# Kernel optimization log

Measured on AMD Instinct MI355X. Metric: run time of the kernel, lower is better.

Reference implementation:

```python
import jax, jax.numpy as jnp
import numpy as np

C = 768      # n_embd
H = 12       # n_head
L = 6        # n_layer (per stack: base and head)
BS = 256     # block_size (per-stream length t)
B = 2        # batch
VU = 512     # vocab_size_up
VD = 512     # vocab_size_down
NM = 438     # n_music


def _ln(x, g, b, eps=1e-5):
    m = jnp.mean(x, -1, keepdims=True)
    v = jnp.mean((x - m) ** 2, -1, keepdims=True)
    return (x - m) * jax.lax.rsqrt(v + eps) * g + b


def _blocks(x, p, mask):
    # p: tuple of 16 stacked [L, ...] param arrays; scan over layers
    def body(x, lp):
        g1, b1, Wq, Bq, Wk, Bk, Wv, Bv, Wo, Bo, g2, b2, Wf, Bf, Wp, Bp = lp
        Bb, T, Cc = x.shape
        D = Cc // H
        h = _ln(x, g1, b1)
        q = (h @ Wq + Bq).reshape(Bb, T, H, D).transpose(0, 2, 1, 3)
        k = (h @ Wk + Bk).reshape(Bb, T, H, D).transpose(0, 2, 1, 3)
        v = (h @ Wv + Bv).reshape(Bb, T, H, D).transpose(0, 2, 1, 3)
        att = jnp.einsum('bhid,bhjd->bhij', q, k) * (1.0 / np.sqrt(D).astype(np.float32))
        att = jnp.where(mask, att, jnp.float32(-1e9))
        att = jax.nn.softmax(att, axis=-1)
        y = jnp.einsum('bhij,bhjd->bhid', att, v).transpose(0, 2, 1, 3).reshape(Bb, T, Cc)
        x = x + y @ Wo + Bo
        h2 = _ln(x, g2, b2)
        x = x + jax.nn.gelu(h2 @ Wf + Bf, approximate=False) @ Wp + Bp
        return x, None
    x, _ = jax.lax.scan(body, x, p)
    return x


def _forward(idx_up, idx_down, cond, tok_emb_up, tok_emb_down, pos_emb, cond_w, cond_b,
             base_p, head_p, ln_f_g, ln_f_b, head_up_w, head_down_w):
    t = idx_up.shape[1]
    te = jnp.concatenate([cond @ cond_w + cond_b, tok_emb_up[idx_up], tok_emb_down[idx_down]], axis=1)
    pe = jnp.concatenate([pos_emb[:, :t], pos_emb[:, BS:BS + t], pos_emb[:, 2 * BS:2 * BS + t]], axis=1)
    x = te + pe  # [B, 3t, C]
    tril = jnp.tril(jnp.ones((t, t), bool))
    mask = jnp.tile(tril, (3, 3))[None, None]  # 3x3 tiled block-causal mask [1,1,3t,3t]
    x = _blocks(x, base_p, mask)
    x = _blocks(x, head_p, mask)
    x = _ln(x, ln_f_g, ln_f_b)
    logits_up = x[:, t:2 * t] @ head_up_w
    logits_down = x[:, 2 * t:3 * t] @ head_down_w
    return logits_up, logits_down


def setup_inputs() -> dict:
    key = jax.random.key(0)
    ks = iter(jax.random.split(key, 100))
    def nrm(shape):
        return 0.02 * jax.random.normal(next(ks), shape, jnp.float32)
    inp = {
        'idx_up': jax.random.randint(next(ks), (B, BS), 0, VU),
        'idx_down': jax.random.randint(next(ks), (B, BS), 0, VD),
        'cond': jax.random.normal(next(ks), (B, BS, NM), jnp.float32),
        'tok_emb_up': nrm((VU, C)),
        'tok_emb_down': nrm((VD, C)),
        'pos_emb': nrm((1, 3 * BS, C)),
        'cond_w': nrm((NM, C)),
        'cond_b': jnp.zeros((C,), jnp.float32),
    }
    for pre in ('base_', 'head_'):
        inp[pre + 'ln1_g'] = jnp.ones((L, C), jnp.float32)
        inp[pre + 'ln1_b'] = jnp.zeros((L, C), jnp.float32)
        inp[pre + 'wq'] = nrm((L, C, C)); inp[pre + 'bq'] = jnp.zeros((L, C), jnp.float32)
        inp[pre + 'wk'] = nrm((L, C, C)); inp[pre + 'bk'] = jnp.zeros((L, C), jnp.float32)
        inp[pre + 'wv'] = nrm((L, C, C)); inp[pre + 'bv'] = jnp.zeros((L, C), jnp.float32)
        inp[pre + 'wo'] = nrm((L, C, C)); inp[pre + 'bo'] = jnp.zeros((L, C), jnp.float32)
        inp[pre + 'ln2_g'] = jnp.ones((L, C), jnp.float32)
        inp[pre + 'ln2_b'] = jnp.zeros((L, C), jnp.float32)
        inp[pre + 'fc_w'] = nrm((L, C, 4 * C)); inp[pre + 'fc_b'] = jnp.zeros((L, 4 * C), jnp.float32)
        inp[pre + 'pr_w'] = nrm((L, 4 * C, C)); inp[pre + 'pr_b'] = jnp.zeros((L, C), jnp.float32)
    inp['ln_f_g'] = jnp.ones((C,), jnp.float32)
    inp['ln_f_b'] = jnp.zeros((C,), jnp.float32)
    inp['head_up_w'] = nrm((C, VU))
    inp['head_down_w'] = nrm((C, VD))
    return inp


def reference(idx_up, idx_down, cond, tok_emb_up, tok_emb_down, pos_emb, cond_w, cond_b,
              base_ln1_g, base_ln1_b, base_wq, base_bq, base_wk, base_bk, base_wv, base_bv,
              base_wo, base_bo, base_ln2_g, base_ln2_b, base_fc_w, base_fc_b, base_pr_w, base_pr_b,
              head_ln1_g, head_ln1_b, head_wq, head_bq, head_wk, head_bk, head_wv, head_bv,
              head_wo, head_bo, head_ln2_g, head_ln2_b, head_fc_w, head_fc_b, head_pr_w, head_pr_b,
              ln_f_g, ln_f_b, head_up_w, head_down_w):
    base_p = (base_ln1_g, base_ln1_b, base_wq, base_bq, base_wk, base_bk, base_wv, base_bv,
              base_wo, base_bo, base_ln2_g, base_ln2_b, base_fc_w, base_fc_b, base_pr_w, base_pr_b)
    head_p = (head_ln1_g, head_ln1_b, head_wq, head_bq, head_wk, head_bk, head_wv, head_bv,
              head_wo, head_bo, head_ln2_g, head_ln2_b, head_fc_w, head_fc_b, head_pr_w, head_pr_b)
    return _forward(idx_up, idx_down, cond, tok_emb_up, tok_emb_down, pos_emb, cond_w, cond_b,
                    base_p, head_p, ln_f_g, ln_f_b, head_up_w, head_down_w)
```

## Files before the change

### kernel.cpp

```cpp
#include <hip/hip_runtime.h>
#include <cmath>

typedef unsigned short u16;
typedef __bf16 bf16x8 __attribute__((ext_vector_type(8)));
typedef float f32x4 __attribute__((ext_vector_type(4)));
typedef float f32x16 __attribute__((ext_vector_type(16)));
typedef u16 u16x4 __attribute__((ext_vector_type(4)));
typedef u16 u16x2 __attribute__((ext_vector_type(2)));
typedef u16 u16x8 __attribute__((ext_vector_type(8)));

#define GLOAD16(g, l) __builtin_amdgcn_global_load_lds( \
    (const __attribute__((address_space(1))) unsigned int*)(g), \
    (__attribute__((address_space(3))) unsigned int*)(l), 16, 0, 0)

__device__ __forceinline__ u16 f2b(float f) {
  unsigned u = __builtin_bit_cast(unsigned, f);
  unsigned r = (u + 0x7fffu + ((u >> 16) & 1u)) >> 16;
  return (u16)r;
}

__device__ __forceinline__ int xcd_swz(int lin, int nwg) {
  int q = nwg >> 3, r = nwg & 7;
  int xcd = lin & 7, idx = lin >> 3;
  return xcd * q + (xcd < r ? xcd : r) + idx;
}

__device__ __forceinline__ void trans_tile(const float* __restrict__ W, u16* __restrict__ Wo,
                                           int K, int N, int Kp, int n0, int k0)
{
  __shared__ float t[32][33];
  int tx = threadIdx.x & 31, ty = threadIdx.x >> 5;
  #pragma unroll
  for (int i = 0; i < 4; ++i) {
    int k = k0 + ty + i * 8;
    t[ty + i * 8][tx] = (k < K) ? W[(long)k * N + n0 + tx] : 0.0f;
  }
  __syncthreads();
  #pragma unroll
  for (int i = 0; i < 2; ++i) {
    int p = threadIdx.x + 256 * i;
    int nl = p >> 4, kk = (p & 15) * 2;
    u16x2 o2; o2[0] = f2b(t[kk][nl]); o2[1] = f2b(t[kk + 1][nl]);
    *(u16x2*)(Wo + (long)(n0 + nl) * Kp + k0 + kk) = o2;
  }
}

__global__ __launch_bounds__(256)
void transall_k(const float* wq0, const float* wk0, const float* wv0, const float* wo0,
                const float* fc0, const float* pr0,
                const float* wq1, const float* wk1, const float* wv1, const float* wo1,
                const float* fc1, const float* pr1,
                const float* hu, const float* hd, const float* cw,
                u16* qkvt, u16* wot, u16* fct, u16* prt, u16* hutd, u16* cwt)
{
  int bid = blockIdx.x;
  const float* src; u16* dst; int K, N, Kp, t, tilesX;
  if (bid < 20736) {
    int l = bid / 1728, local = bid - l * 1728;
    int s = l / 6, li = l - s * 6;
    if (local < 432) {
      int p = local / 144; t = local - p * 144;
      const float* base = (p == 0) ? (s ? wq1 : wq0) : (p == 1) ? (s ? wk1 : wk0) : (s ? wv1 : wv0);
      src = base + (size_t)li * 768 * 768;
      dst = qkvt + (size_t)l * 2304 * 768 + (size_t)p * 768 * 768;
      K = 768; N = 768; Kp = 768; tilesX = 12;
    } else if (local < 576) {
      t = local - 432;
      src = (s ? wo1 : wo0) + (size_t)li * 768 * 768;
      dst = wot + (size_t)l * 768 * 768;
      K = 768; N = 768; Kp = 768; tilesX = 12;
    } else if (local < 1152) {
      t = local - 576;
      src = (s ? fc1 : fc0) + (size_t)li * 768 * 3072;
      dst = fct + (size_t)l * 3072 * 768;
      K = 768; N = 3072; Kp = 768; tilesX = 48;
    } else {
      t = local - 1152;
      src = (s ? pr1 : pr0) + (size_t)li * 3072 * 768;
      dst = prt + (size_t)l * 768 * 3072;
      K = 3072; N = 768; Kp = 3072; tilesX = 12;
    }
  } else {
    int e = bid - 20736;
    if (e < 96)       { t = e;       src = hu; dst = hutd;             K = 768; N = 512; Kp = 768; tilesX = 8; }
    else if (e < 192) { t = e - 96;  src = hd; dst = hutd + 512 * 768; K = 768; N = 512; Kp = 768; tilesX = 8; }
    else              { t = e - 192; src = cw; dst = cwt;              K = 438; N = 768; Kp = 448; tilesX = 12; }
  }
  int n0 = (t % tilesX) * 64, k0 = (t / tilesX) * 64;

  __shared__ float tl[64][65];
  const int tid = threadIdx.x;
  const int c4 = (tid & 15) * 4, rbase = tid >> 4;
  #pragma unroll
  for (int p = 0; p < 4; ++p) {
    int r = rbase + p * 16;
    int k = k0 + r;
    float4 v = make_float4(0.0f, 0.0f, 0.0f, 0.0f);
    if (k < K) v = *(const float4*)(src + (long)k * N + n0 + c4);
    tl[r][c4] = v.x; tl[r][c4 + 1] = v.y; tl[r][c4 + 2] = v.z; tl[r][c4 + 3] = v.w;
  }
  __syncthreads();
  const int kg = (tid & 7) * 8, nbase = tid >> 3;
  #pragma unroll
  for (int p = 0; p < 2; ++p) {
    int n = nbase + p * 32;
    u16x8 pk;
    #pragma unroll
    for (int j = 0; j < 8; ++j) pk[j] = f2b(tl[kg + j][n]);
    *(u16x8*)(dst + (long)(n0 + n) * Kp + k0 + kg) = pk;
  }
}

__global__ __launch_bounds__(256)
void transw_k(const float* __restrict__ W, u16* __restrict__ Wt,
              int K, int N, int Kp, long sIn, long sOut)
{
  int l = blockIdx.z;
  trans_tile(W + (long)l * sIn, Wt + (long)l * sOut, K, N, Kp, blockIdx.x * 32, blockIdx.y * 32);
}

__global__ __launch_bounds__(256)
void prep_k(const float* bq0, const float* bk0, const float* bv0,
            const float* bq1, const float* bk1, const float* bv1, float* qkvb,
            const float* cond, u16* cbf,
            const int* iu, const int* idn, const float* teu, const float* ted,
            const float* pe, float* x)
{
  int idx = blockIdx.x * 256 + threadIdx.x;
  if (idx < 27648) {
    int c = idx % 2304, l = idx / 2304;
    int st = l / 6, li = l % 6;
    const float* src = (c < 768) ? (st ? bq1 : bq0) : (c < 1536) ? (st ? bk1 : bk0) : (st ? bv1 : bv0);
    qkvb[idx] = src[li * 768 + (c % 768)];
  } else if (idx < 27648 + 57344) {
    int i2 = idx - 27648;
    int r = i2 / 112, kk = (i2 - r * 112) * 4;
    u16x4 pk;
    #pragma unroll
    for (int i = 0; i < 4; ++i) { int k = kk + i; pk[i] = f2b(k < 438 ? cond[r * 438 + k] : 0.0f); }
    *(u16x4*)(cbf + r * 448 + kk) = pk;
  } else if (idx < 27648 + 57344 + 196608) {
    int i3 = idx - 27648 - 57344;
    int c4 = i3 % 192; int rest = i3 / 192;
    int tt = rest % 512; int b = rest / 512;
    int i = tt & 255; int s = tt >> 8;
    int tok = s ? idn[b * 256 + i] : iu[b * 256 + i];
    const float4* src = (const float4*)(s ? (ted + (long)tok * 768) : (teu + (long)tok * 768));
    int prow = 256 + s * 256 + i;
    float4 pv = ((const float4*)(pe + (long)prow * 768))[c4];
    float4 sv = src[c4];
    float4 ov; ov.x = sv.x + pv.x; ov.y = sv.y + pv.y; ov.z = sv.z + pv.z; ov.w = sv.w + pv.w;
    ((float4*)(x + ((long)b * 768 + prow) * 768))[c4] = ov;
  }
}

template<int S, bool WX>
__global__ __launch_bounds__(256)
void lnred_k(const float* __restrict__ xin, const float* __restrict__ P,
             const float* __restrict__ bias, const float* __restrict__ gg,
             const float* __restrict__ bb, float* __restrict__ xout,
             u16* __restrict__ h)
{
  int row = blockIdx.x * 4 + (threadIdx.x >> 6);
  int lane = threadIdx.x & 63;
  long base = (long)row * 768;
  const float4* xr4 = (const float4*)(xin + base);
  float4 v[3]; float s = 0.0f;
  #pragma unroll
  for (int j = 0; j < 3; ++j) {
    int f = lane + 64 * j;
    float4 val = xr4[f];
    if (S > 0) {
      float4 bv = ((const float4*)bias)[f];
      val.x += bv.x; val.y += bv.y; val.z += bv.z; val.w += bv.w;
      #pragma unroll
      for (int si = 0; si < S; ++si) {
        float4 pv = ((const float4*)(P + (long)si * 1179648 + base))[f];
        val.x += pv.x; val.y += pv.y; val.z += pv.z; val.w += pv.w;
      }
    }
    if (WX) ((float4*)(xout + base))[f] = val;
    v[j] = val; s += val.x + val.y + val.z + val.w;
  }
  #pragma unroll
  for (int d = 1; d < 64; d <<= 1) s += __shfl_xor(s, d);
  float mean = s * (1.0f / 768.0f);
  float s2 = 0.0f;
  #pragma unroll
  for (int j = 0; j < 3; ++j) {
    float dx = v[j].x - mean, dy = v[j].y - mean, dz = v[j].z - mean, dw = v[j].w - mean;
    s2 += dx * dx + dy * dy + dz * dz + dw * dw;
  }
  #pragma unroll
  for (int d = 1; d < 64; d <<= 1) s2 += __shfl_xor(s2, d);
  float rstd = rsqrtf(s2 * (1.0f / 768.0f) + 1e-5f);
  u16* orow = h + base;
  #pragma unroll
  for (int j = 0; j < 3; ++j) {
    int f = lane + 64 * j;
    float4 gv = ((const float4*)gg)[f];
    float4 bv2 = ((const float4*)bb)[f];
    u16x4 pk;
    pk[0] = f2b((v[j].x - mean) * rstd * gv.x + bv2.x);
    pk[1] = f2b((v[j].y - mean) * rstd * gv.y + bv2.y);
    pk[2] = f2b((v[j].z - mean) * rstd * gv.z + bv2.z);
    pk[3] = f2b((v[j].w - mean) * rstd * gv.w + bv2.w);
    *(u16x4*)(orow + 4 * f) = pk;
  }
}

__global__ __launch_bounds__(256)
void headred_k(const float* __restrict__ HP, float* __restrict__ out)
{
  int i4 = blockIdx.x * 256 + threadIdx.x;
  int st = i4 >> 16, loc = i4 & 65535;
  int r = loc >> 7, c4 = loc & 127;
  const float4* basep = (const float4*)HP + (long)r * 256 + st * 128 + c4;
  float4 a = basep[0], b = basep[131072], c = basep[2 * 131072], d = basep[3 * 131072];
  float4 rr; rr.x = a.x + b.x + c.x + d.x; rr.y = a.y + b.y + c.y + d.y;
  rr.z = a.z + b.z + c.z + d.z; rr.w = a.w + b.w + c.w + d.w;
  ((float4*)out)[i4] = rr;
}

#define EPI_PLAIN 0
#define EPI_PE    1
#define EPI_QKV   2
#define EPI_GELU  4
#define EPI_PART  5
#define EPI_HEAD  6

template<int BM, int BN, int WM, int WN, int EPI, bool BIAS>
__global__ __launch_bounds__(256)
void gemm_k(const u16* __restrict__ A, const u16* __restrict__ Bt, const float* __restrict__ bias,
            float* outf, u16* outb, u16* qb, u16* kb, u16* vT, const float* aux,
            int M, int N, int Ks, int lda, int ldb, int ldc,
            int astr, int aoff, int cstr, int coff, int pstr)
{
  constexpr int NWC = BN / WN;
  constexpr int NT  = (BM / WM) * NWC * 64;
  constexpr int LCH = (BM + BN) * 8;
  constexpr int LPT = LCH / NT;
  constexpr int MR = WM / 32, NR = WN / 32;
  __shared__ alignas(16) u16 Sl[2][(BM + BN) * 64];

  const int tid = threadIdx.x;
  const int gx = gridDim.x, gy = gridDim.y;
  const int nwg = gx * gy * gridDim.z;
  const int lin = (blockIdx.z * gy + blockIdx.y) * gx + blockIdx.x;
  const int wg = xcd_swz(lin, nwg);
  const int bx = wg % gx, t1g = wg / gx;
  const int by = t1g % gy, bz = t1g / gy;
  const int m0 = bx * BM, n0 = by * BN;
  const int koff = bz * Ks;
  const int lane = tid & 63, w = tid >> 6;
  const int l31 = lane & 31, hl = lane >> 5;
  const int wr = w / NWC, wc = w % NWC;
  int aoffE = aoff;
  if constexpr (EPI == EPI_HEAD) aoffE += (by >= (int)(gy >> 1)) ? 256 : 0;

  const u16* gp[LPT]; int lbase[LPT];
  #pragma unroll
  for (int j = 0; j < LPT; ++j) {
    int c = tid + NT * j;
    int slot = c & 7;
    if (c < BM * 8) {
      int row = c >> 3;
      int se = (slot ^ (row & 7)) * 8;
      int am = m0 + row;
      gp[j] = A + (long)((am >> 8) * astr + aoffE + (am & 255)) * lda + koff + se;
    } else {
      int rb = c - BM * 8;
      int row = rb >> 3;
      int se = (slot ^ (row & 7)) * 8;
      gp[j] = Bt + (long)(n0 + row) * ldb + koff + se;
    }
    lbase[j] = w * 512 + NT * 8 * j;
  }

  int offA[4][MR], offB[4][NR];
  #pragma unroll
  for (int kst = 0; kst < 4; ++kst) {
    int s = 2 * kst + hl;
    #pragma unroll
    for (int mi = 0; mi < MR; ++mi) {
      int r = wr * WM + mi * 32 + l31;
      offA[kst][mi] = r * 128 + ((s ^ (r & 7)) << 4);
    }
    #pragma unroll
    for (int ni = 0; ni < NR; ++ni) {
      int r = wc * WN + ni * 32 + l31;
      offB[kst][ni] = BM * 128 + r * 128 + ((s ^ (r & 7)) << 4);
    }
  }

  f32x16 acc[MR][NR];
  #pragma unroll
  for (int mi = 0; mi < MR; ++mi)
  #pragma unroll
  for (int ni = 0; ni < NR; ++ni) acc[mi][ni] = f32x16{};

  auto STAGE = [&](int kt, int buf) {
    #pragma unroll
    for (int j = 0; j < LPT; ++j) GLOAD16(gp[j] + kt, &Sl[buf][lbase[j]]);
  };
  auto COMPUTE = [&](int buf) {
    const char* Sb = (const char*)&Sl[buf][0];
    #pragma unroll
    for (int kst = 0; kst < 4; ++kst) {
      bf16x8 a[MR], b[NR];
      #pragma unroll
      for (int mi = 0; mi < MR; ++mi) a[mi] = *(const bf16x8*)(Sb + offA[kst][mi]);
      #pragma unroll
      for (int ni = 0; ni < NR; ++ni) b[ni] = *(const bf16x8*)(Sb + offB[kst][ni]);
      #pragma unroll
      for (int mi = 0; mi < MR; ++mi)
      #pragma unroll
      for (int ni = 0; ni < NR; ++ni)
        acc[mi][ni] = __builtin_amdgcn_mfma_f32_32x32x16_bf16(a[mi], b[ni], acc[mi][ni], 0, 0, 0);
    }
  };

  const int nIter = Ks >> 6;
  STAGE(0, 0);
  if (nIter > 1) STAGE(64, 1);
  for (int t = 0; t < nIter; ++t) {
    if (t + 1 < nIter) {
      if constexpr (LPT == 8)      asm volatile("s_waitcnt vmcnt(8)" ::: "memory");
      else if constexpr (LPT == 6) asm volatile("s_waitcnt vmcnt(6)" ::: "memory");
      else                         asm volatile("s_waitcnt vmcnt(4)" ::: "memory");
    } else {
      asm volatile("s_waitcnt vmcnt(0)" ::: "memory");
    }
    __builtin_amdgcn_s_barrier();
    COMPUTE(t & 1);
    if (t + 2 < nIter) {
      __builtin_amdgcn_s_barrier();
      STAGE((t + 2) << 6, t & 1);
    }
  }

  #pragma unroll
  for (int mi = 0; mi < MR; ++mi)
  #pragma unroll
  for (int ni = 0; ni < NR; ++ni) {
    f32x16 a = acc[mi][ni];
    int col = n0 + wc * WN + ni * 32 + l31;
    float bv = BIAS ? bias[col] : 0.0f;
    int mlb = m0 + wr * WM + mi * 32 + 4 * hl;
    if constexpr (EPI == EPI_QKV) {
      if (col >= 1536) {
        int c2 = col - 1536, hh = c2 >> 6, dd = c2 & 63;
        #pragma unroll
        for (int q = 0; q < 4; ++q) {
          int t0r = mlb + 8 * q;
          int bb2 = t0r >= 768 ? 1 : 0;
          int t0 = t0r - bb2 * 768;
          u16x4 pk;
          #pragma unroll
          for (int r = 0; r < 4; ++r) pk[r] = f2b(a[4 * q + r] + bv);
          *(u16x4*)(vT + (long)((bb2 * 12 + hh) * 64 + dd) * 768 + t0) = pk;
        }
      } else {
        u16* dst = (col < 768) ? (qb + col) : (kb + (col - 768));
        #pragma unroll
        for (int q = 0; q < 4; ++q)
        #pragma unroll
        for (int r = 0; r < 4; ++r) {
          int row = mlb + 8 * q + r;
          dst[(long)row * 768] = f2b(a[4 * q + r] + bv);
        }
      }
    } else {
      #pragma unroll
      for (int q = 0; q < 4; ++q)
      #pragma unroll
      for (int r = 0; r < 4; ++r) {
        int rg = mlb + 8 * q + r;
        long crow = (long)(rg >> 8) * cstr + coff + (rg & 255);
        float v = a[4 * q + r] + bv;
        if (EPI == EPI_PLAIN)      outf[crow * ldc + col] = v;
        else if (EPI == EPI_PE)    outf[crow * ldc + col] = v + aux[(long)(rg & 255) * 768 + col];
        else if (EPI == EPI_PART || EPI == EPI_HEAD)
                                   outf[(long)bz * pstr + (long)rg * ldc + col] = v;
        else if (EPI == EPI_GELU)  outb[crow * ldc + col] = f2b(0.5f * v * (1.0f + erff(v * 0.70710678f)));
      }
    }
  }
}

#define MFMA_BF16 __builtin_amdgcn_mfma_f32_16x16x32_bf16
__global__ __launch_bounds__(128)
void attn_k(const u16* __restrict__ qb, const u16* __restrict__ kb,
            const u16* __restrict__ vT, u16* __restrict__ y)
{
  __shared__ alignas(16) u16 Kl[3 * 4096];
  __shared__ alignas(16) u16 Vl[3 * 4096];
  __shared__ alignas(16) u16 Pl[2][16 * 72];
  const int gx = gridDim.x, gy = gridDim.y;
  const int nwg = gx * gy;
  const int lin = blockIdx.y * gx + blockIdx.x;
  const int wg = xcd_swz(lin, nwg);
  const int qt = wg % gx, bh = wg / gx;
  const int b = bh / 12, h = bh - b * 12;
  const int tid = threadIdx.x, w = tid >> 6, lane = tid & 63, l15 = lane & 15, g = lane >> 4;
  const int qrow = qt * 32 + w * 16 + l15;
  const int qm = qrow & 255;
  const int q0 = (qt * 32) & 255;
  const unsigned nw4 = (q0 >> 6) + 1;
  const int niter = 3 * nw4;
  const u16* qp = qb + (long)(b * 768 + qrow) * 768 + h * 64;
  bf16x8 qf0 = *(const bf16x8*)(qp + 8 * g);
  bf16x8 qf1 = *(const bf16x8*)(qp + 32 + 8 * g);
  f32x4 O0{}, O1{}, O2{}, O3{};
  float m_run = -1e30f, l_run = 0.0f;

  const u16* kp[4]; const u16* vp[4]; int ldsb[4];
  #pragma unroll
  for (int j = 0; j < 4; ++j) {
    int i = tid + 128 * j;
    int r = i >> 3, sl = ((i & 7) ^ (r & 7)) * 8;
    kp[j] = kb + (long)(b * 768 + r) * 768 + h * 64 + sl;
    vp[j] = vT + (long)(bh * 64 + r) * 768 + sl;
    ldsb[j] = (w + 2 * j) * 512;
  }

  auto STAGE = [&](int kt, int q) {
    u16* kd = Kl + q * 4096; u16* vd = Vl + q * 4096;
    #pragma unroll
    for (int j = 0; j < 4; ++j) GLOAD16(kp[j] + (long)kt * 64 * 768, kd + ldsb[j]);
    #pragma unroll
    for (int j = 0; j < 4; ++j) GLOAD16(vp[j] + kt * 64, vd + ldsb[j]);
  };
  auto MAP = [&](int it) {
    unsigned sb = (unsigned)it / nw4;
    return (int)(sb * 4 + ((unsigned)it - sb * nw4));
  };

  STAGE(MAP(0), 0);
  STAGE(MAP(1), 1);
  int cur = 0;
  for (int it = 0; it < niter; ++it) {
    if (it < niter - 1) asm volatile("s_waitcnt vmcnt(8)" ::: "memory");
    else                asm volatile("s_waitcnt vmcnt(0)" ::: "memory");
    __builtin_amdgcn_s_barrier();
    if (it + 2 < niter) STAGE(MAP(it + 2), cur == 0 ? 2 : cur - 1);
    const int kt = MAP(it);
    const char* Kb = (const char*)Kl + cur * 8192;
    const char* Vb = (const char*)Vl + cur * 8192;

    f32x4 s0{}, s1{}, s2{}, s3{};
    #pragma unroll
    for (int ks = 0; ks < 2; ++ks) {
      bf16x8 qf = ks ? qf1 : qf0;
      int sb = ((4 * ks + g) ^ (l15 & 7)) << 4;
      bf16x8 k0 = *(const bf16x8*)(Kb + (0  + l15) * 128 + sb);
      bf16x8 k1 = *(const bf16x8*)(Kb + (16 + l15) * 128 + sb);
      bf16x8 k2 = *(const bf16x8*)(Kb + (32 + l15) * 128 + sb);
      bf16x8 k3 = *(const bf16x8*)(Kb + (48 + l15) * 128 + sb);
      s0 = MFMA_BF16(k0, qf, s0, 0, 0, 0);
      s1 = MFMA_BF16(k1, qf, s1, 0, 0, 0);
      s2 = MFMA_BF16(k2, qf, s2, 0, 0, 0);
      s3 = MFMA_BF16(k3, qf, s3, 0, 0, 0);
    }
    float sv[16]; float tm = -1e30f;
    #pragma unroll
    for (int mt = 0; mt < 4; ++mt) {
      f32x4 sm4 = (mt == 0) ? s0 : (mt == 1) ? s1 : (mt == 2) ? s2 : s3;
      #pragma unroll
      for (int r = 0; r < 4; ++r) {
        int kg = kt * 64 + mt * 16 + 4 * g + r;
        float val = ((kg & 255) <= qm) ? sm4[r] * 0.125f : -1e30f;
        sv[mt * 4 + r] = val; tm = fmaxf(tm, val);
      }
    }
    tm = fmaxf(tm, __shfl_xor(tm, 16));
    tm = fmaxf(tm, __shfl_xor(tm, 32));
    float mn = fmaxf(m_run, tm);
    float alpha = __expf(m_run - mn);
    float ps = 0.0f; u16 pb16[16];
    #pragma unroll
    for (int j = 0; j < 16; ++j) {
      float p = (sv[j] <= -1e29f) ? 0.0f : __expf(sv[j] - mn);
      ps += p; pb16[j] = f2b(p);
    }
    ps += __shfl_xor(ps, 16); ps += __shfl_xor(ps, 32);
    l_run = l_run * alpha + ps; m_run = mn;
    float a0 = __shfl(alpha, 4 * g + 0);
    float a1 = __shfl(alpha, 4 * g + 1);
    float a2 = __shfl(alpha, 4 * g + 2);
    float a3 = __shfl(alpha, 4 * g + 3);
    #pragma unroll
    for (int mt = 0; mt < 4; ++mt) {
      u16x4 pk; pk[0] = pb16[4*mt]; pk[1] = pb16[4*mt+1]; pk[2] = pb16[4*mt+2]; pk[3] = pb16[4*mt+3];
      *(u16x4*)((char*)&Pl[w][0] + l15 * 144 + mt * 32 + 8 * g) = pk;
    }
    O0[0] *= a0; O0[1] *= a1; O0[2] *= a2; O0[3] *= a3;
    O1[0] *= a0; O1[1] *= a1; O1[2] *= a2; O1[3] *= a3;
    O2[0] *= a0; O2[1] *= a1; O2[2] *= a2; O2[3] *= a3;
    O3[0] *= a0; O3[1] *= a1; O3[2] *= a2; O3[3] *= a3;
    asm volatile("s_waitcnt lgkmcnt(0)" ::: "memory");
    __builtin_amdgcn_sched_barrier(0);
    #pragma unroll
    for (int ks = 0; ks < 2; ++ks) {
      bf16x8 pf = *(const bf16x8*)((const char*)&Pl[w][0] + l15 * 144 + 64 * ks + 16 * g);
      int sb = ((4 * ks + g) ^ (l15 & 7)) << 4;
      bf16x8 v0 = *(const bf16x8*)(Vb + (0  + l15) * 128 + sb);
      bf16x8 v1 = *(const bf16x8*)(Vb + (16 + l15) * 128 + sb);
      bf16x8 v2 = *(const bf16x8*)(Vb + (32 + l15) * 128 + sb);
      bf16x8 v3 = *(const bf16x8*)(Vb + (48 + l15) * 128 + sb);
      O0 = MFMA_BF16(pf, v0, O0, 0, 0, 0);
      O1 = MFMA_BF16(pf, v1, O1, 0, 0, 0);
      O2 = MFMA_BF16(pf, v2, O2, 0, 0, 0);
      O3 = MFMA_BF16(pf, v3, O3, 0, 0, 0);
    }
    cur = (cur == 2) ? 0 : cur + 1;
  }
  float n0i = 1.0f / __shfl(l_run, 4 * g + 0);
  float n1i = 1.0f / __shfl(l_run, 4 * g + 1);
  float n2i = 1.0f / __shfl(l_run, 4 * g + 2);
  float n3i = 1.0f / __shfl(l_run, 4 * g + 3);
  long yr = (long)(b * 768 + qt * 32 + w * 16 + 4 * g);
  #pragma unroll
  for (int ni = 0; ni < 4; ++ni) {
    f32x4 Ov = (ni == 0) ? O0 : (ni == 1) ? O1 : (ni == 2) ? O2 : O3;
    int c = h * 64 + ni * 16 + l15;
    y[(yr + 0) * 768 + c] = f2b(Ov[0] * n0i);
    y[(yr + 1) * 768 + c] = f2b(Ov[1] * n1i);
    y[(yr + 2) * 768 + c] = f2b(Ov[2] * n2i);
    y[(yr + 3) * 768 + c] = f2b(Ov[3] * n3i);
  }
}

extern "C" void kernel_launch(void* const* d_in, const int* in_sizes, int n_in,
                              void* d_out, int out_size, void* d_ws, size_t ws_size,
                              hipStream_t stream)
{
  (void)in_sizes; (void)n_in; (void)out_size;
  auto F = [&](int i){ return (const float*)d_in[i]; };
  const int* idx_up = (const int*)d_in[0];
  const int* idx_dn = (const int*)d_in[1];
  const float* cond = F(2);
  const float* teu = F(3);
  const float* ted = F(4);
  const float* pe  = F(5);
  const float* cw  = F(6);
  const float* cb  = F(7);
  float* outp = (float*)d_out;
  char* ws = (char*)d_ws;

  size_t o = 0;
  auto take = [&](size_t bytes){ void* p = ws + o; o += bytes; return p; };
  float* x    = (float*)take(4718592);
  u16*   h    = (u16*)take(2359296);
  u16*   qbuf = (u16*)take(2359296);
  u16*   kbuf = (u16*)take(2359296);
  u16*   vT   = (u16*)take(2359296);
  u16*   y    = (u16*)take(2359296);
  u16*   fca  = (u16*)take(9437184);
  u16*   xf   = (u16*)take(2359296);
  u16*   cbf  = (u16*)take(458752);
  float* qkvb = (float*)take(110592);
  u16*   hutd = (u16*)take(1572864);
  u16*   cwt  = (u16*)take(688128);
  float* P1   = (float*)take(9437184);
  float* P2   = (float*)take(9437184);
  float* HP   = (float*)take(8388608);
  const size_t WL = 14155776;
  bool up = (ws_size >= o + 12 * WL);
  size_t nsl = up ? 12 : 1;
  u16* qkvt = (u16*)(ws + o);
  u16* wot  = qkvt + nsl * 2304 * 768;
  u16* fct  = wot  + nsl * 768 * 768;
  u16* prt  = fct  + nsl * 3072 * 768;

  auto trans = [&](const float* src, u16* dst, int K, int N, int Kp, long sIn, long sOut, int nz){
    transw_k<<<dim3(N / 32, Kp / 32, nz), dim3(256), 0, stream>>>(src, dst, K, N, Kp, sIn, sOut);
  };

  if (up) {
    transall_k<<<dim3(21012), dim3(256), 0, stream>>>(
        F(10), F(12), F(14), F(16), F(20), F(22),
        F(26), F(28), F(30), F(32), F(36), F(38),
        F(42), F(43), cw,
        qkvt, wot, fct, prt, hutd, cwt);
  } else {
    trans(F(42), hutd, 768, 512, 768, 0, 0, 1);
    trans(F(43), hutd + 512 * 768, 768, 512, 768, 0, 0, 1);
    trans(cw,    cwt, 438, 768, 448, 0, 0, 1);
  }
  prep_k<<<dim3(1100), dim3(256), 0, stream>>>(
      F(11), F(13), F(15), F(27), F(29), F(31), qkvb,
      cond, cbf, idx_up, idx_dn, teu, ted, pe, x);
  gemm_k<64, 64, 32, 32, EPI_PE, true><<<dim3(8, 12, 1), dim3(256), 0, stream>>>(cbf, cwt, cb,
      x, nullptr, nullptr, nullptr, nullptr, pe,
      512, 768, 448, 448, 448, 768, 256, 0, 768, 0, 0);

  for (int l = 0; l < 12; ++l) {
    int s = l / 6, li = l % 6;
    u16* qkvt_l = qkvt + (up ? (size_t)l : 0) * 2304 * 768;
    u16* wot_l  = wot  + (up ? (size_t)l : 0) * 768 * 768;
    u16* fct_l  = fct  + (up ? (size_t)l : 0) * 3072 * 768;
    u16* prt_l  = prt  + (up ? (size_t)l : 0) * 768 * 3072;
    if (!up) {
      for (int p = 0; p < 3; ++p)
        trans(F(8 + 16*s + 2 + 2*p) + (size_t)li*768*768, qkvt_l + (size_t)p*768*768, 768, 768, 768, 0, 0, 1);
      trans(F(8 + 16*s + 8)  + (size_t)li*768*768,  wot_l, 768, 768, 768, 0, 0, 1);
      trans(F(8 + 16*s + 12) + (size_t)li*768*3072, fct_l, 768, 3072, 768, 0, 0, 1);
      trans(F(8 + 16*s + 14) + (size_t)li*3072*768, prt_l, 3072, 768, 3072, 0, 0, 1);
    }
    if (l == 0) {
      lnred_k<0, false><<<dim3(384), dim3(256), 0, stream>>>(x, nullptr, nullptr,
          F(8+16*s+0) + (size_t)li*768, F(8+16*s+1) + (size_t)li*768, nullptr, h);
    } else {
      int ps = (l - 1) / 6, pli = (l - 1) % 6;
      lnred_k<2, true><<<dim3(384), dim3(256), 0, stream>>>(x, P2,
          F(8+16*ps+15) + (size_t)pli*768,
          F(8+16*s+0) + (size_t)li*768, F(8+16*s+1) + (size_t)li*768, x, h);
    }
    gemm_k<128, 64, 32, 64, EPI_QKV, true><<<dim3(12, 36, 1), dim3(256), 0, stream>>>(h, qkvt_l, qkvb + (size_t)l*2304,
        nullptr, nullptr, qbuf, kbuf, vT, nullptr,
        1536, 2304, 768, 768, 768, 768, 256, 0, 256, 0, 0);
    attn_k<<<dim3(24, 24), dim3(128), 0, stream>>>(qbuf, kbuf, vT, y);
    gemm_k<128, 64, 32, 64, EPI_PART, false><<<dim3(12, 12, 2), dim3(256), 0, stream>>>(y, wot_l, nullptr,
        P1, nullptr, nullptr, nullptr, nullptr, nullptr,
        1536, 768, 384, 768, 768, 768, 256, 0, 256, 0, 1179648);
    lnred_k<2, true><<<dim3(384), dim3(256), 0, stream>>>(x, P1,
        F(8+16*s+9) + (size_t)li*768,
        F(8+16*s+10) + (size_t)li*768, F(8+16*s+11) + (size_t)li*768, x, h);
    gemm_k<128, 64, 32, 64, EPI_GELU, true><<<dim3(12, 48, 1), dim3(256), 0, stream>>>(h, fct_l, F(8+16*s+13) + (size_t)li*3072,
        nullptr, fca, nullptr, nullptr, nullptr, nullptr,
        1536, 3072, 768, 768, 768, 3072, 256, 0, 256, 0, 0);
    gemm_k<128, 64, 32, 64, EPI_PART, false><<<dim3(12, 12, 2), dim3(256), 0, stream>>>(fca, prt_l, nullptr,
        P2, nullptr, nullptr, nullptr, nullptr, nullptr,
        1536, 768, 1536, 3072, 3072, 768, 256, 0, 256, 0, 1179648);
  }
  lnred_k<2, false><<<dim3(384), dim3(256), 0, stream>>>(x, P2,
      F(8+16*1+15) + (size_t)5*768, F(40), F(41), nullptr, xf);
  gemm_k<64, 64, 32, 32, EPI_HEAD, false><<<dim3(8, 16, 4), dim3(256), 0, stream>>>(xf, hutd, nullptr,
      HP, nullptr, nullptr, nullptr, nullptr, nullptr,
      512, 1024, 192, 768, 768, 1024, 768, 256, 256, 0, 524288);
  headred_k<<<dim3(512), dim3(256), 0, stream>>>(HP, outp);
}
```

Baseline: 1.227 ms.

## Fuse layernorm into following GEMMs via cooperative launch with grid sync

Merges each layernorm/residual-reduce kernel with the GEMM that consumes it into a single cooperative kernel. Each workgroup first normalizes rows, then a grid-wide sync, then runs the GEMM tile body. This cuts separate kernel launches and gaps between them. In exchange it adds the cost of a grid barrier, and cooperative launch requires all 432/576/512 workgroups to be co-resident, which constrains occupancy.

Result: slower. 3.078 ms (+150.8%).

```diff
diff --git a/kernel.cpp b/kernel.cpp
--- a/kernel.cpp
+++ b/kernel.cpp
@@ -1,5 +1,8 @@
 #include <hip/hip_runtime.h>
+#include <hip/hip_cooperative_groups.h>
 #include <cmath>
+
+namespace cg = cooperative_groups;
 
 typedef unsigned short u16;
 typedef __bf16 bf16x8 __attribute__((ext_vector_type(8)));
@@ -155,13 +158,11 @@
 }
 
 template<int S, bool WX>
-__global__ __launch_bounds__(256)
-void lnred_k(const float* __restrict__ xin, const float* __restrict__ P,
-             const float* __restrict__ bias, const float* __restrict__ gg,
-             const float* __restrict__ bb, float* __restrict__ xout,
-             u16* __restrict__ h)
-{
-  int row = blockIdx.x * 4 + (threadIdx.x >> 6);
+__device__ __forceinline__ void ln_row(int row, const float* __restrict__ xin,
+                                       const float* __restrict__ P, const float* __restrict__ bias,
+                                       const float* __restrict__ gg, const float* __restrict__ bb,
+                                       float* __restrict__ xout, u16* __restrict__ h)
+{
   int lane = threadIdx.x & 63;
   long base = (long)row * 768;
   const float4* xr4 = (const float4*)(xin + base);
@@ -230,23 +231,21 @@
 #define EPI_HEAD  6
 
 template<int BM, int BN, int WM, int WN, int EPI, bool BIAS>
-__global__ __launch_bounds__(256)
-void gemm_k(const u16* __restrict__ A, const u16* __restrict__ Bt, const float* __restrict__ bias,
-            float* outf, u16* outb, u16* qb, u16* kb, u16* vT, const float* aux,
-            int M, int N, int Ks, int lda, int ldb, int ldc,
-            int astr, int aoff, int cstr, int coff, int pstr)
+__device__ __forceinline__
+void gemm_body(u16* Sl, int lin, int gx, int gy, int nwg,
+               const u16* __restrict__ A, const u16* __restrict__ Bt, const float* __restrict__ bias,
+               float* outf, u16* outb, u16* qb, u16* kb, u16* vT, const float* aux,
+               int M, int N, int Ks, int lda, int ldb, int ldc,
+               int astr, int aoff, int cstr, int coff, int pstr)
 {
   constexpr int NWC = BN / WN;
   constexpr int NT  = (BM / WM) * NWC * 64;
   constexpr int LCH = (BM + BN) * 8;
   constexpr int LPT = LCH / NT;
   constexpr int MR = WM / 32, NR = WN / 32;
-  __shared__ alignas(16) u16 Sl[2][(BM + BN) * 64];
+  constexpr int BUFE = (BM + BN) * 64;
 
   const int tid = threadIdx.x;
-  const int gx = gridDim.x, gy = gridDim.y;
-  const int nwg = gx * gy * gridDim.z;
-  const int lin = (blockIdx.z * gy + blockIdx.y) * gx + blockIdx.x;
   const int wg = xcd_swz(lin, nwg);
   const int bx = wg % gx, t1g = wg / gx;
   const int by = t1g % gy, bz = t1g / gy;
@@ -256,7 +255,7 @@
   const int l31 = lane & 31, hl = lane >> 5;
   const int wr = w / NWC, wc = w % NWC;
   int aoffE = aoff;
-  if constexpr (EPI == EPI_HEAD) aoffE += (by >= (int)(gy >> 1)) ? 256 : 0;
+  if constexpr (EPI == EPI_HEAD) aoffE += (by >= (gy >> 1)) ? 256 : 0;
 
   const u16* gp[LPT]; int lbase[LPT];
   #pragma unroll
@@ -301,10 +300,10 @@
 
   auto STAGE = [&](int kt, int buf) {
     #pragma unroll
-    for (int j = 0; j < LPT; ++j) GLOAD16(gp[j] + kt, &Sl[buf][lbase[j]]);
+    for (int j = 0; j < LPT; ++j) GLOAD16(gp[j] + kt, Sl + buf * BUFE + lbase[j]);
   };
   auto COMPUTE = [&](int buf) {
-    const char* Sb = (const char*)&Sl[buf][0];
+    const char* Sb = (const char*)Sl + buf * BUFE * 2;
     #pragma unroll
     for (int kst = 0; kst < 4; ++kst) {
       bf16x8 a[MR], b[NR];
@@ -388,6 +387,65 @@
   }
 }
 
+template<int BM, int BN, int WM, int WN, int EPI, bool BIAS>
+__global__ __launch_bounds__(256)
+void gemm_k(const u16* __restrict__ A, const u16* __restrict__ Bt, const float* __restrict__ bias,
+            float* outf, u16* outb, u16* qb, u16* kb, u16* vT, const float* aux,
+            int M, int N, int Ks, int lda, int ldb, int ldc,
+            int astr, int aoff, int cstr, int coff, int pstr)
+{
+  __shared__ alignas(16) u16 Sl[2][(BM + BN) * 64];
+  const int gx = gridDim.x, gy = gridDim.y;
+  const int nwg = gx * gy * gridDim.z;
+  const int lin = (blockIdx.z * gy + blockIdx.y) * gx + blockIdx.x;
+  gemm_body<BM, BN, WM, WN, EPI, BIAS>(&Sl[0][0], lin, gx, gy, nwg,
+      A, Bt, bias, outf, outb, qb, kb, vT, aux,
+      M, N, Ks, lda, ldb, ldc, astr, aoff, cstr, coff, pstr);
+}
+
+template<int S, bool WX>
+__global__ __launch_bounds__(256, 3)
+void coop_qkv_k(const float* xin, const float* P, const float* pbias,
+                const float* gg, const float* bb, float* xout, u16* h,
+                const u16* Bt, const float* qbias, u16* qb, u16* kb, u16* vT)
+{
+  __shared__ alignas(16) u16 Sl[2][(128 + 64) * 64];
+  int wid = blockIdx.x * 4 + (threadIdx.x >> 6);
+  if (wid < 1536) ln_row<S, WX>(wid, xin, P, pbias, gg, bb, xout, h);
+  cg::this_grid().sync();
+  gemm_body<128, 64, 32, 64, EPI_QKV, true>(&Sl[0][0], blockIdx.x, 12, 36, 432,
+      h, Bt, qbias, nullptr, nullptr, qb, kb, vT, nullptr,
+      1536, 2304, 768, 768, 768, 768, 256, 0, 256, 0, 0);
+}
+
+__global__ __launch_bounds__(256, 3)
+void coop_fc_k(const float* xin, const float* P, const float* pbias,
+               const float* gg, const float* bb, float* xout, u16* h,
+               const u16* Bt, const float* fcbias, u16* fca)
+{
+  __shared__ alignas(16) u16 Sl[2][(128 + 64) * 64];
+  int wid = blockIdx.x * 4 + (threadIdx.x >> 6);
+  if (wid < 1536) ln_row<2, true>(wid, xin, P, pbias, gg, bb, xout, h);
+  cg::this_grid().sync();
+  gemm_body<128, 64, 32, 64, EPI_GELU, true>(&Sl[0][0], blockIdx.x, 12, 48, 576,
+      h, Bt, fcbias, nullptr, fca, nullptr, nullptr, nullptr, nullptr,
+      1536, 3072, 768, 768, 768, 3072, 256, 0, 256, 0, 0);
+}
+
+__global__ __launch_bounds__(256, 3)
+void coop_head_k(const float* xin, const float* P, const float* pbias,
+                 const float* gg, const float* bb, u16* xf,
+                 const u16* Bt, float* HP)
+{
+  __shared__ alignas(16) u16 Sl[2][(64 + 64) * 64];
+  int wid = blockIdx.x * 4 + (threadIdx.x >> 6);
+  if (wid < 1536) ln_row<2, false>(wid, xin, P, pbias, gg, bb, nullptr, xf);
+  cg::this_grid().sync();
+  gemm_body<64, 64, 32, 32, EPI_HEAD, false>(&Sl[0][0], blockIdx.x, 8, 16, 512,
+      xf, Bt, nullptr, HP, nullptr, nullptr, nullptr, nullptr, nullptr,
+      512, 1024, 192, 768, 768, 1024, 768, 256, 256, 0, 524288);
+}
+
 #define MFMA_BF16 __builtin_amdgcn_mfma_f32_16x16x32_bf16
 __global__ __launch_bounds__(128)
 void attn_k(const u16* __restrict__ qb, const u16* __restrict__ kb,
@@ -608,36 +666,47 @@
       trans(F(8 + 16*s + 12) + (size_t)li*768*3072, fct_l, 768, 3072, 768, 0, 0, 1);
       trans(F(8 + 16*s + 14) + (size_t)li*3072*768, prt_l, 3072, 768, 3072, 0, 0, 1);
     }
+    const float* g1 = F(8+16*s+0) + (size_t)li*768;
+    const float* b1 = F(8+16*s+1) + (size_t)li*768;
+    const float* qbias = qkvb + (size_t)l*2304;
     if (l == 0) {
-      lnred_k<0, false><<<dim3(384), dim3(256), 0, stream>>>(x, nullptr, nullptr,
-          F(8+16*s+0) + (size_t)li*768, F(8+16*s+1) + (size_t)li*768, nullptr, h);
+      const float* pb = nullptr;
+      void* a1[] = {(void*)&x, (void*)&P2, (void*)&pb, (void*)&g1, (void*)&b1,
+                    (void*)&x, (void*)&h, (void*)&qkvt_l, (void*)&qbias,
+                    (void*)&qbuf, (void*)&kbuf, (void*)&vT};
+      hipLaunchCooperativeKernel((const void*)coop_qkv_k<0, false>, dim3(432), dim3(256), a1, 0, stream);
     } else {
       int ps = (l - 1) / 6, pli = (l - 1) % 6;
-      lnred_k<2, true><<<dim3(384), dim3(256), 0, stream>>>(x, P2,
-          F(8+16*ps+15) + (size_t)pli*768,
-          F(8+16*s+0) + (size_t)li*768, F(8+16*s+1) + (size_t)li*768, x, h);
-    }
-    gemm_k<128, 64, 32, 64, EPI_QKV, true><<<dim3(12, 36, 1), dim3(256), 0, stream>>>(h, qkvt_l, qkvb + (size_t)l*2304,
-        nullptr, nullptr, qbuf, kbuf, vT, nullptr,
-        1536, 2304, 768, 768, 768, 768, 256, 0, 256, 0, 0);
+      const float* pb = F(8+16*ps+15) + (size_t)pli*768;
+      void* a1[] = {(void*)&x, (void*)&P2, (void*)&pb, (void*)&g1, (void*)&b1,
+                    (void*)&x, (void*)&h, (void*)&qkvt_l, (void*)&qbias,
+                    (void*)&qbuf, (void*)&kbuf, (void*)&vT};
+      hipLaunchCooperativeKernel((const void*)coop_qkv_k<2, true>, dim3(432), dim3(256), a1, 0, stream);
+    }
     attn_k<<<dim3(24, 24), dim3(128), 0, stream>>>(qbuf, kbuf, vT, y);
     gemm_k<128, 64, 32, 64, EPI_PART, false><<<dim3(12, 12, 2), dim3(256), 0, stream>>>(y, wot_l, nullptr,
         P1, nullptr, nullptr, nullptr, nullptr, nullptr,
         1536, 768, 384, 768, 768, 768, 256, 0, 256, 0, 1179648);
-    lnred_k<2, true><<<dim3(384), dim3(256), 0, stream>>>(x, P1,
-        F(8+16*s+9) + (size_t)li*768,
-        F(8+16*s+10) + (size_t)li*768, F(8+16*s+11) + (size_t)li*768, x, h);
-    gemm_k<128, 64, 32, 64, EPI_GELU, true><<<dim3(12, 48, 1), dim3(256), 0, stream>>>(h, fct_l, F(8+16*s+13) + (size_t)li*3072,
-        nullptr, fca, nullptr, nullptr, nullptr, nullptr,
-        1536, 3072, 768, 768, 768, 3072, 256, 0, 256, 0, 0);
+    {
+      const float* bo = F(8+16*s+9) + (size_t)li*768;
+      const float* g2 = F(8+16*s+10) + (size_t)li*768;
+      const float* b2 = F(8+16*s+11) + (size_t)li*768;
+      const float* fcb = F(8+16*s+13) + (size_t)li*3072;
+      void* a2[] = {(void*)&x, (void*)&P1, (void*)&bo, (void*)&g2, (void*)&b2,
+                    (void*)&x, (void*)&h, (void*)&fct_l, (void*)&fcb, (void*)&fca};
+      hipLaunchCooperativeKernel((const void*)coop_fc_k, dim3(576), dim3(256), a2, 0, stream);
+    }
     gemm_k<128, 64, 32, 64, EPI_PART, false><<<dim3(12, 12, 2), dim3(256), 0, stream>>>(fca, prt_l, nullptr,
         P2, nullptr, nullptr, nullptr, nullptr, nullptr,
         1536, 768, 1536, 3072, 3072, 768, 256, 0, 256, 0, 1179648);
   }
-  lnred_k<2, false><<<dim3(384), dim3(256), 0, stream>>>(x, P2,
-      F(8+16*1+15) + (size_t)5*768, F(40), F(41), nullptr, xf);
-  gemm_k<64, 64, 32, 32, EPI_HEAD, false><<<dim3(8, 16, 4), dim3(256), 0, stream>>>(xf, hutd, nullptr,
-      HP, nullptr, nullptr, nullptr, nullptr, nullptr,
-      512, 1024, 192, 768, 768, 1024, 768, 256, 256, 0, 524288);
+  {
+    const float* pb = F(8+16*1+15) + (size_t)5*768;
+    const float* gf = F(40);
+    const float* bf = F(41);
+    void* a3[] = {(void*)&x, (void*)&P2, (void*)&pb, (void*)&gf, (void*)&bf,
+                  (void*)&xf, (void*)&hutd, (void*)&HP};
+    hipLaunchCooperativeKernel((const void*)coop_head_k, dim3(512), dim3(256), a3, 0, stream);
+  }
   headred_k<<<dim3(512), dim3(256), 0, stream>>>(HP, outp);
 }
```
